# Optimization experiments

Measured on AMD Instinct MI355X. Metric: run time of the kernel, lower is better.

## Reference

```python
import jax, jax.numpy as jnp
import numpy as np

jax.config.update("jax_enable_x64", True)  # hash ids exceed int32 range

N = 2_000_000
C = 32
IGNORE_INDEX = -1
BOUNDARY_SCALE = 3.0
GAMMA = 1.0
LOSS_WEIGHT = 1.0
EPS = 1e-6


def setup_inputs() -> dict:
    key = jax.random.key(0)
    k1, k2, k3, k4, k5 = jax.random.split(key, 5)
    pred = jax.random.normal(k1, (N, C), dtype=jnp.float32)
    target = jax.random.randint(k2, (N,), 0, C, dtype=jnp.int64)
    grid_coord = jax.random.randint(k3, (N, 3), 0, 128, dtype=jnp.int64)
    normal = jax.random.normal(k4, (N, 3), dtype=jnp.float32)
    batch = jax.random.randint(k5, (N,), 0, 8, dtype=jnp.int64)
    return {"pred": pred, "target": target, "grid_coord": grid_coord,
            "normal": normal, "batch": batch}


def _l2_normalize(x, eps=EPS):
    # F.normalize: x / max(||x||, eps)
    nrm = jnp.linalg.norm(x, axis=-1, keepdims=True)
    return x / jnp.maximum(nrm, eps)


def _hash_grid_coord(grid_coord, batch):
    gc = grid_coord.astype(jnp.int64)
    base1 = jnp.int64(1000003)
    base2 = jnp.int64(10007)
    vid = gc[:, 0] * base1 * base1 + gc[:, 1] * base1 + gc[:, 2]
    vid = vid + batch.astype(jnp.int64) * (base1 * base1 * base1 + base2)
    return vid


def reference(pred, target, grid_coord, normal, batch):
    valid = target != IGNORE_INDEX                         # (N,)
    vm = valid.astype(pred.dtype)                          # float mask
    n_pts = pred.shape[0]

    voxel_id = _hash_grid_coord(grid_coord, batch)         # (N,) int64
    # Compact voxel ids -> segment indices (equivalent to unique+inverse)
    _, inv = jnp.unique(voxel_id, return_inverse=True, size=n_pts, fill_value=jnp.int64(0))
    inv = inv.reshape(-1)

    # scatter_mean of normals over voxels (invalid points masked out,
    # matching the original's pre-filtering by `valid`)
    seg_sum = jax.ops.segment_sum(normal * vm[:, None], inv, num_segments=n_pts)  # (N,3)
    seg_cnt = jax.ops.segment_sum(vm, inv, num_segments=n_pts)                    # (N,)
    voxel_mean_n = seg_sum / jnp.maximum(seg_cnt, 1.0)[:, None]
    voxel_mean_n = _l2_normalize(voxel_mean_n)

    mean_n_per_point = voxel_mean_n[inv]                   # gather back to points
    n_v = _l2_normalize(normal)

    cos = jnp.clip(jnp.sum(n_v * mean_n_per_point, axis=-1), -1.0, 1.0)
    diff = 1.0 - cos                                       # boundary strength

    big = jnp.asarray(jnp.inf, diff.dtype)
    d_min = jnp.min(jnp.where(valid, diff, big))
    d_max = jnp.max(jnp.where(valid, diff, -big))
    diff_norm = jnp.clip((diff - d_min) / (d_max - d_min + EPS), 0.0, 1.0)

    w = 1.0 + BOUNDARY_SCALE * diff_norm ** GAMMA
    w = jax.lax.stop_gradient(w)                           # detach_weight=True

    # per-point cross entropy on valid points
    logp = jax.nn.log_softmax(pred, axis=-1)
    tgt_safe = jnp.where(valid, target, 0)
    ce = -jnp.take_along_axis(logp, tgt_safe[:, None], axis=1)[:, 0]

    loss = jnp.sum(ce * w * vm) / jnp.maximum(jnp.sum(vm), 1.0)
    return loss * LOSS_WEIGHT
```

## Files before the change

kernel.cpp:

```cpp
#include <hip/hip_runtime.h>
#include <hip/hip_bf16.h>
#include <stdint.h>


#define IGNORE_INDEX (-1)

constexpr long long B1 = 1000003LL;
constexpr long long B2 = 10007LL;
constexpr long long B1SQ = B1 * B1;
constexpr long long BMUL = B1 * B1 * B1 + B2;
constexpr unsigned long long EMPTY_KEY = 0xFFFFFFFFFFFFFFFFULL;

__device__ __forceinline__ unsigned long long mix64(unsigned long long x) {
    x ^= x >> 33; x *= 0xff51afd7ed558ccdULL;
    x ^= x >> 33; x *= 0xc4ceb9fe1a85ec53ULL;
    x ^= x >> 33;
    return x;
}

__global__ void k_scatter(const int* __restrict__ tgt,
                          const int* __restrict__ gc,
                          const float* __restrict__ nrm,
                          const int* __restrict__ bat,
                          unsigned long long* __restrict__ keys,
                          float* __restrict__ acc,
                          int* __restrict__ slots,
                          int n, unsigned mask) {
    int i = blockIdx.x * blockDim.x + threadIdx.x;
    if (i >= n) return;
    long long vid = (long long)gc[3 * i] * B1SQ
                  + (long long)gc[3 * i + 1] * B1
                  + (long long)gc[3 * i + 2]
                  + (long long)bat[i] * BMUL;
    unsigned long long key = (unsigned long long)vid;
    unsigned slot = (unsigned)(mix64(key)) & mask;
    while (true) {
        unsigned long long prev = atomicCAS(&keys[slot], EMPTY_KEY, key);
        if (prev == EMPTY_KEY || prev == key) break;
        slot = (slot + 1) & mask;
    }
    slots[i] = (int)slot;
    if (tgt[i] != IGNORE_INDEX) {
        float* a = acc + (size_t)slot * 4;
        atomicAdd(a + 0, nrm[3 * i]);
        atomicAdd(a + 1, nrm[3 * i + 1]);
        atomicAdd(a + 2, nrm[3 * i + 2]);
        atomicAdd(a + 3, 1.0f);
    }
}

__global__ void k_diff(const int* __restrict__ tgt,
                       const float* __restrict__ nrm,
                       const float4* __restrict__ acc,
                       const int* __restrict__ slots,
                       float* __restrict__ diff,
                       unsigned* __restrict__ gmm,
                       int n) {
    int i = blockIdx.x * blockDim.x + threadIdx.x;
    float d = 0.0f;
    bool valid = false;
    if (i < n) {
        float4 a = acc[slots[i]];
        float c = fmaxf(a.w, 1.0f);
        float mx = a.x / c, my = a.y / c, mz = a.z / c;
        float mlen = sqrtf(mx * mx + my * my + mz * mz);
        float md = fmaxf(mlen, 1e-6f);
        mx /= md; my /= md; mz /= md;
        float nx = nrm[3 * i], ny = nrm[3 * i + 1], nz = nrm[3 * i + 2];
        float nlen = sqrtf(nx * nx + ny * ny + nz * nz);
        float nd = fmaxf(nlen, 1e-6f);
        nx /= nd; ny /= nd; nz /= nd;
        float cosv = nx * mx + ny * my + nz * mz;
        cosv = fminf(1.0f, fmaxf(-1.0f, cosv));
        d = 1.0f - cosv;
        diff[i] = d;
        valid = (tgt[i] != IGNORE_INDEX);
    }
    float vmin = valid ? d : INFINITY;
    float vmax = valid ? d : -INFINITY;
    #pragma unroll
    for (int o = 32; o > 0; o >>= 1) {
        vmin = fminf(vmin, __shfl_down(vmin, o, 64));
        vmax = fmaxf(vmax, __shfl_down(vmax, o, 64));
    }
    __shared__ float smin[4], smax[4];
    int wid = threadIdx.x >> 6;
    if ((threadIdx.x & 63) == 0) { smin[wid] = vmin; smax[wid] = vmax; }
    __syncthreads();
    if (threadIdx.x == 0) {
        float bmin = smin[0], bmax = smax[0];
        int nw = blockDim.x >> 6;
        for (int w = 1; w < nw; ++w) { bmin = fminf(bmin, smin[w]); bmax = fmaxf(bmax, smax[w]); }
        if (bmin != INFINITY) atomicMin(&gmm[0], __float_as_uint(bmin));
        if (bmax >= 0.0f)     atomicMax(&gmm[1], __float_as_uint(bmax));
    }
}

__global__ void k_ce(const float* __restrict__ pred,
                     const int* __restrict__ tgt,
                     const float* __restrict__ diff,
                     const unsigned* __restrict__ gmm,
                     double* __restrict__ gsum,
                     int n) {
    int i = blockIdx.x * blockDim.x + threadIdx.x;
    float wce = 0.0f, vmv = 0.0f;
    if (i < n) {
        int t = tgt[i];
        if (t != IGNORE_INDEX) {
            float dmin = __uint_as_float(gmm[0]);
            float dmax = __uint_as_float(gmm[1]);
            float dn = (diff[i] - dmin) / (dmax - dmin + 1e-6f);
            dn = fminf(1.0f, fmaxf(0.0f, dn));
            float w = 1.0f + 3.0f * dn;
            const float4* rp = (const float4*)(pred + (size_t)i * 32);
            float4 v[8];
            #pragma unroll
            for (int j = 0; j < 8; ++j) v[j] = rp[j];
            float m = v[0].x;
            #pragma unroll
            for (int j = 0; j < 8; ++j)
                m = fmaxf(m, fmaxf(fmaxf(v[j].x, v[j].y), fmaxf(v[j].z, v[j].w)));
            float s = 0.0f;
            #pragma unroll
            for (int j = 0; j < 8; ++j)
                s += expf(v[j].x - m) + expf(v[j].y - m) + expf(v[j].z - m) + expf(v[j].w - m);
            float pt = ((const float*)rp)[t];
            float ce = -(pt - m - logf(s));
            wce = ce * w;
            vmv = 1.0f;
        }
    }
    #pragma unroll
    for (int o = 32; o > 0; o >>= 1) {
        wce += __shfl_down(wce, o, 64);
        vmv += __shfl_down(vmv, o, 64);
    }
    __shared__ float swce[4], svm[4];
    int wid = threadIdx.x >> 6;
    if ((threadIdx.x & 63) == 0) { swce[wid] = wce; svm[wid] = vmv; }
    __syncthreads();
    if (threadIdx.x == 0) {
        float bw = swce[0], bv = svm[0];
        int nw = blockDim.x >> 6;
        for (int w = 1; w < nw; ++w) { bw += swce[w]; bv += svm[w]; }
        atomicAdd(&gsum[0], (double)bw);
        atomicAdd(&gsum[1], (double)bv);
    }
}

__global__ void k_final(const double* __restrict__ gsum, float* __restrict__ out) {
    if (threadIdx.x == 0 && blockIdx.x == 0) {
        double denom = gsum[1] > 1.0 ? gsum[1] : 1.0;
        out[0] = (float)(gsum[0] / denom);
    }
}

extern "C" void kernel_launch(void* const* d_in, const int* in_sizes, int n_in,
                              void* d_out, int out_size, void* d_ws, size_t ws_size,
                              hipStream_t stream) {
    const float* pred   = (const float*)d_in[0];
    const int*   target = (const int*)d_in[1];
    const int*   gc     = (const int*)d_in[2];
    const float* normal = (const float*)d_in[3];
    const int*   bat    = (const int*)d_in[4];
    const int n = in_sizes[1];

    size_t tsize = (size_t)1 << 22;
    while (tsize > ((size_t)1 << 20) &&
           tsize * 24 + (size_t)n * 8 + 256 > ws_size)
        tsize >>= 1;

    char* p = (char*)d_ws;
    unsigned long long* keys = (unsigned long long*)p; p += tsize * 8;
    float* acc = (float*)p;                            p += tsize * 16;
    int* slots = (int*)p;                              p += (size_t)n * 4;
    float* diff = (float*)p;                           p += (size_t)n * 4;
    p = (char*)(((uintptr_t)p + 15) & ~(uintptr_t)15);
    unsigned* gmm = (unsigned*)p;
    double* gsum = (double*)(p + 16);

    hipMemsetAsync(keys, 0xFF, tsize * 8, stream);
    hipMemsetAsync(acc, 0, tsize * 16, stream);
    hipMemsetAsync(gmm, 0x7F, 4, stream);
    hipMemsetAsync((char*)gmm + 4, 0, 28, stream);

    const int blk = 256;
    const int grid = (n + blk - 1) / blk;
    const unsigned mask = (unsigned)(tsize - 1);

    k_scatter<<<grid, blk, 0, stream>>>(target, gc, normal, bat, keys, acc, slots, n, mask);
    k_diff<<<grid, blk, 0, stream>>>(target, normal, (const float4*)acc, slots, diff, gmm, n);
    k_ce<<<grid, blk, 0, stream>>>(pred, target, diff, gmm, gsum, n);
    k_final<<<1, 1, 0, stream>>>(gsum, (float*)d_out);
}
```

Baseline: 1.205 ms.

## Fuse diff and CE kernels via linear weight decomposition with packed 32-bit hash table

The boundary weight is linear in diff, so the loss becomes S1 + 3*(S2 - dmin*S1)/range. That lets the diff, min/max and cross-entropy passes merge into one kernel, with the normalisation done in k_final. The hash table now uses 32-bit packed keys (7-bit coordinates plus batch) stored in the same 16-byte record as the normal sums, and the count and mean division are dropped because only the direction is needed. This removes a full pass over pred-sized data, the diff buffer and one kernel launch. The price is reliance on coordinates below 128 and batch below 8, plus possible cancellation in the algebraic rewrite.

```diff
diff --git a/kernel.cpp b/kernel.cpp
--- a/kernel.cpp
+++ b/kernel.cpp
@@ -4,114 +4,75 @@
 
 
 #define IGNORE_INDEX (-1)
+constexpr unsigned EMPTY32 = 0xFFFFFFFFu;
 
-constexpr long long B1 = 1000003LL;
-constexpr long long B2 = 10007LL;
-constexpr long long B1SQ = B1 * B1;
-constexpr long long BMUL = B1 * B1 * B1 + B2;
-constexpr unsigned long long EMPTY_KEY = 0xFFFFFFFFFFFFFFFFULL;
+__device__ __forceinline__ unsigned hash24(unsigned k) {
+    k *= 0x9E3779B1u; k ^= k >> 16; k *= 0x85EBCA6Bu; k ^= k >> 13;
+    return k;
+}
 
-__device__ __forceinline__ unsigned long long mix64(unsigned long long x) {
-    x ^= x >> 33; x *= 0xff51afd7ed558ccdULL;
-    x ^= x >> 33; x *= 0xc4ceb9fe1a85ec53ULL;
-    x ^= x >> 33;
-    return x;
+__global__ void k_init(uint4* __restrict__ tab, int tsize) {
+    int i = blockIdx.x * blockDim.x + threadIdx.x;
+    if (i < tsize) tab[i] = make_uint4(EMPTY32, 0u, 0u, 0u);
 }
 
 __global__ void k_scatter(const int* __restrict__ tgt,
                           const int* __restrict__ gc,
                           const float* __restrict__ nrm,
                           const int* __restrict__ bat,
-                          unsigned long long* __restrict__ keys,
-                          float* __restrict__ acc,
+                          float* __restrict__ tab,
                           int* __restrict__ slots,
                           int n, unsigned mask) {
     int i = blockIdx.x * blockDim.x + threadIdx.x;
     if (i >= n) return;
-    long long vid = (long long)gc[3 * i] * B1SQ
-                  + (long long)gc[3 * i + 1] * B1
-                  + (long long)gc[3 * i + 2]
-                  + (long long)bat[i] * BMUL;
-    unsigned long long key = (unsigned long long)vid;
-    unsigned slot = (unsigned)(mix64(key)) & mask;
+    if (tgt[i] == IGNORE_INDEX) return;
+    unsigned gx = (unsigned)gc[3 * i];
+    unsigned gy = (unsigned)gc[3 * i + 1];
+    unsigned gz = (unsigned)gc[3 * i + 2];
+    unsigned b  = (unsigned)bat[i];
+    unsigned key = gx | (gy << 7) | (gz << 14) | (b << 21);
+    float nx = nrm[3 * i], ny = nrm[3 * i + 1], nz = nrm[3 * i + 2];
+    unsigned slot = hash24(key) & mask;
     while (true) {
-        unsigned long long prev = atomicCAS(&keys[slot], EMPTY_KEY, key);
-        if (prev == EMPTY_KEY || prev == key) break;
+        unsigned prev = atomicCAS((unsigned*)(tab + (size_t)slot * 4), EMPTY32, key);
+        if (prev == EMPTY32 || prev == key) break;
         slot = (slot + 1) & mask;
     }
     slots[i] = (int)slot;
-    if (tgt[i] != IGNORE_INDEX) {
-        float* a = acc + (size_t)slot * 4;
-        atomicAdd(a + 0, nrm[3 * i]);
-        atomicAdd(a + 1, nrm[3 * i + 1]);
-        atomicAdd(a + 2, nrm[3 * i + 2]);
-        atomicAdd(a + 3, 1.0f);
-    }
+    float* r = tab + (size_t)slot * 4;
+    atomicAdd(r + 1, nx);
+    atomicAdd(r + 2, ny);
+    atomicAdd(r + 3, nz);
 }
 
-__global__ void k_diff(const int* __restrict__ tgt,
-                       const float* __restrict__ nrm,
-                       const float4* __restrict__ acc,
-                       const int* __restrict__ slots,
-                       float* __restrict__ diff,
-                       unsigned* __restrict__ gmm,
-                       int n) {
+__global__ void k_fused(const float* __restrict__ pred,
+                        const int* __restrict__ tgt,
+                        const float* __restrict__ nrm,
+                        const float4* __restrict__ tab,
+                        const int* __restrict__ slots,
+                        unsigned* __restrict__ gmm,
+                        double* __restrict__ gsum,
+                        int n) {
     int i = blockIdx.x * blockDim.x + threadIdx.x;
+    float s1 = 0.0f, s2 = 0.0f, s3 = 0.0f;
     float d = 0.0f;
     bool valid = false;
     if (i < n) {
-        float4 a = acc[slots[i]];
-        float c = fmaxf(a.w, 1.0f);
-        float mx = a.x / c, my = a.y / c, mz = a.z / c;
-        float mlen = sqrtf(mx * mx + my * my + mz * mz);
-        float md = fmaxf(mlen, 1e-6f);
-        mx /= md; my /= md; mz /= md;
-        float nx = nrm[3 * i], ny = nrm[3 * i + 1], nz = nrm[3 * i + 2];
-        float nlen = sqrtf(nx * nx + ny * ny + nz * nz);
-        float nd = fmaxf(nlen, 1e-6f);
-        nx /= nd; ny /= nd; nz /= nd;
-        float cosv = nx * mx + ny * my + nz * mz;
-        cosv = fminf(1.0f, fmaxf(-1.0f, cosv));
-        d = 1.0f - cosv;
-        diff[i] = d;
-        valid = (tgt[i] != IGNORE_INDEX);
-    }
-    float vmin = valid ? d : INFINITY;
-    float vmax = valid ? d : -INFINITY;
-    #pragma unroll
-    for (int o = 32; o > 0; o >>= 1) {
-        vmin = fminf(vmin, __shfl_down(vmin, o, 64));
-        vmax = fmaxf(vmax, __shfl_down(vmax, o, 64));
-    }
-    __shared__ float smin[4], smax[4];
-    int wid = threadIdx.x >> 6;
-    if ((threadIdx.x & 63) == 0) { smin[wid] = vmin; smax[wid] = vmax; }
-    __syncthreads();
-    if (threadIdx.x == 0) {
-        float bmin = smin[0], bmax = smax[0];
-        int nw = blockDim.x >> 6;
-        for (int w = 1; w < nw; ++w) { bmin = fminf(bmin, smin[w]); bmax = fmaxf(bmax, smax[w]); }
-        if (bmin != INFINITY) atomicMin(&gmm[0], __float_as_uint(bmin));
-        if (bmax >= 0.0f)     atomicMax(&gmm[1], __float_as_uint(bmax));
-    }
-}
-
-__global__ void k_ce(const float* __restrict__ pred,
-                     const int* __restrict__ tgt,
-                     const float* __restrict__ diff,
-                     const unsigned* __restrict__ gmm,
-                     double* __restrict__ gsum,
-                     int n) {
-    int i = blockIdx.x * blockDim.x + threadIdx.x;
-    float wce = 0.0f, vmv = 0.0f;
-    if (i < n) {
         int t = tgt[i];
         if (t != IGNORE_INDEX) {
-            float dmin = __uint_as_float(gmm[0]);
-            float dmax = __uint_as_float(gmm[1]);
-            float dn = (diff[i] - dmin) / (dmax - dmin + 1e-6f);
-            dn = fminf(1.0f, fmaxf(0.0f, dn));
-            float w = 1.0f + 3.0f * dn;
+            valid = true;
+            float4 rec = tab[slots[i]];
+            float mx = rec.y, my = rec.z, mz = rec.w;
+            float mlen = sqrtf(mx * mx + my * my + mz * mz);
+            float md = fmaxf(mlen, 1e-6f);
+            mx /= md; my /= md; mz /= md;
+            float nx = nrm[3 * i], ny = nrm[3 * i + 1], nz = nrm[3 * i + 2];
+            float nlen = sqrtf(nx * nx + ny * ny + nz * nz);
+            float nd = fmaxf(nlen, 1e-6f);
+            nx /= nd; ny /= nd; nz /= nd;
+            float cosv = nx * mx + ny * my + nz * mz;
+            cosv = fminf(1.0f, fmaxf(-1.0f, cosv));
+            d = 1.0f - cosv;
             const float4* rp = (const float4*)(pred + (size_t)i * 32);
             float4 v[8];
             #pragma unroll
@@ -126,32 +87,55 @@
                 s += expf(v[j].x - m) + expf(v[j].y - m) + expf(v[j].z - m) + expf(v[j].w - m);
             float pt = ((const float*)rp)[t];
             float ce = -(pt - m - logf(s));
-            wce = ce * w;
-            vmv = 1.0f;
+            s1 = ce;
+            s2 = ce * d;
+            s3 = 1.0f;
         }
     }
+    float vmin = valid ? d : INFINITY;
+    float vmax = valid ? d : -INFINITY;
     #pragma unroll
     for (int o = 32; o > 0; o >>= 1) {
-        wce += __shfl_down(wce, o, 64);
-        vmv += __shfl_down(vmv, o, 64);
+        s1 += __shfl_down(s1, o, 64);
+        s2 += __shfl_down(s2, o, 64);
+        s3 += __shfl_down(s3, o, 64);
+        vmin = fminf(vmin, __shfl_down(vmin, o, 64));
+        vmax = fmaxf(vmax, __shfl_down(vmax, o, 64));
     }
-    __shared__ float swce[4], svm[4];
+    __shared__ float sh[5][4];
     int wid = threadIdx.x >> 6;
-    if ((threadIdx.x & 63) == 0) { swce[wid] = wce; svm[wid] = vmv; }
+    if ((threadIdx.x & 63) == 0) {
+        sh[0][wid] = s1; sh[1][wid] = s2; sh[2][wid] = s3;
+        sh[3][wid] = vmin; sh[4][wid] = vmax;
+    }
     __syncthreads();
     if (threadIdx.x == 0) {
-        float bw = swce[0], bv = svm[0];
         int nw = blockDim.x >> 6;
-        for (int w = 1; w < nw; ++w) { bw += swce[w]; bv += svm[w]; }
-        atomicAdd(&gsum[0], (double)bw);
-        atomicAdd(&gsum[1], (double)bv);
+        float b1 = sh[0][0], b2 = sh[1][0], b3 = sh[2][0];
+        float bmin = sh[3][0], bmax = sh[4][0];
+        for (int w = 1; w < nw; ++w) {
+            b1 += sh[0][w]; b2 += sh[1][w]; b3 += sh[2][w];
+            bmin = fminf(bmin, sh[3][w]); bmax = fmaxf(bmax, sh[4][w]);
+        }
+        if (bmin != INFINITY) atomicMin(&gmm[0], __float_as_uint(bmin));
+        if (bmax >= 0.0f)     atomicMax(&gmm[1], __float_as_uint(bmax));
+        atomicAdd(&gsum[0], (double)b1);
+        atomicAdd(&gsum[1], (double)b2);
+        atomicAdd(&gsum[2], (double)b3);
     }
 }
 
-__global__ void k_final(const double* __restrict__ gsum, float* __restrict__ out) {
+__global__ void k_final(const unsigned* __restrict__ gmm,
+                        const double* __restrict__ gsum,
+                        float* __restrict__ out) {
     if (threadIdx.x == 0 && blockIdx.x == 0) {
-        double denom = gsum[1] > 1.0 ? gsum[1] : 1.0;
-        out[0] = (float)(gsum[0] / denom);
+        float dmin = __uint_as_float(gmm[0]);
+        float dmax = __uint_as_float(gmm[1]);
+        float range = dmax - dmin + 1e-6f;
+        double S1 = gsum[0], S2 = gsum[1], S3 = gsum[2];
+        double wce = S1 + 3.0 * (S2 - (double)dmin * S1) / (double)range;
+        double denom = S3 > 1.0 ? S3 : 1.0;
+        out[0] = (float)(wce / denom);
     }
 }
 
@@ -166,30 +150,27 @@
     const int n = in_sizes[1];
 
     size_t tsize = (size_t)1 << 22;
-    while (tsize > ((size_t)1 << 20) &&
-           tsize * 24 + (size_t)n * 8 + 256 > ws_size)
+    while (tsize > ((size_t)1 << 21) &&
+           tsize * 16 + (size_t)n * 4 + 256 > ws_size)
         tsize >>= 1;
 
     char* p = (char*)d_ws;
-    unsigned long long* keys = (unsigned long long*)p; p += tsize * 8;
-    float* acc = (float*)p;                            p += tsize * 16;
-    int* slots = (int*)p;                              p += (size_t)n * 4;
-    float* diff = (float*)p;                           p += (size_t)n * 4;
+    float* tab = (float*)p;                  p += tsize * 16;
+    int* slots = (int*)p;                    p += (size_t)n * 4;
     p = (char*)(((uintptr_t)p + 15) & ~(uintptr_t)15);
     unsigned* gmm = (unsigned*)p;
     double* gsum = (double*)(p + 16);
 
-    hipMemsetAsync(keys, 0xFF, tsize * 8, stream);
-    hipMemsetAsync(acc, 0, tsize * 16, stream);
+    hipMemsetAsync(gmm, 0, 64, stream);
     hipMemsetAsync(gmm, 0x7F, 4, stream);
-    hipMemsetAsync((char*)gmm + 4, 0, 28, stream);
 
     const int blk = 256;
     const int grid = (n + blk - 1) / blk;
     const unsigned mask = (unsigned)(tsize - 1);
 
-    k_scatter<<<grid, blk, 0, stream>>>(target, gc, normal, bat, keys, acc, slots, n, mask);
-    k_diff<<<grid, blk, 0, stream>>>(target, normal, (const float4*)acc, slots, diff, gmm, n);
-    k_ce<<<grid, blk, 0, stream>>>(pred, target, diff, gmm, gsum, n);
-    k_final<<<1, 1, 0, stream>>>(gsum, (float*)d_out);
+    k_init<<<(int)((tsize + blk - 1) / blk), blk, 0, stream>>>((uint4*)tab, (int)tsize);
+    k_scatter<<<grid, blk, 0, stream>>>(target, gc, normal, bat, tab, slots, n, mask);
+    k_fused<<<grid, blk, 0, stream>>>(pred, target, normal, (const float4*)tab, slots,
+                                      gmm, gsum, n);
+    k_final<<<1, 1, 0, stream>>>(gmm, gsum, (float*)d_out);
 }
```

Result: no change. 1.186 ms (-1.5%).
